# Kernel optimization log

Measured on AMD Instinct MI355X. Metric: run time of the kernel, lower is better.

The kernel has to match this reference:

```python
import jax, jax.numpy as jnp
import numpy as np

B, V, D, H, A = 512, 64, 32, 64, 8  # batch, num_vars, input_dim, hidden, out_dim
E = V * (V - 1)
HALF_LOG_2PI = 0.5 * float(np.log(2.0 * np.pi))
LOG2 = float(np.log(2.0))


def setup_inputs() -> dict:
    key = jax.random.key(0)
    ks = jax.random.split(key, 16)
    adj = np.ones((V, V)) - np.eye(V)
    send, recv = np.where(adj)
    s = 0.05
    return {
        "inputs": jax.random.normal(ks[0], (B, V, D), jnp.float32),
        "edges": jax.random.uniform(ks[1], (B, E, 2), jnp.float32),
        "m1_w": jax.random.normal(ks[2], (2 * D, H), jnp.float32) * s,
        "m1_b": jax.random.normal(ks[3], (H,), jnp.float32) * s,
        "m2_w": jax.random.normal(ks[4], (H, H), jnp.float32) * s,
        "m2_b": jax.random.normal(ks[5], (H,), jnp.float32) * s,
        "fc1_w": jax.random.normal(ks[6], (D + H, H), jnp.float32) * s,
        "fc1_b": jax.random.normal(ks[7], (H,), jnp.float32) * s,
        "fc2_w": jax.random.normal(ks[8], (H, H), jnp.float32) * s,
        "fc2_b": jax.random.normal(ks[9], (H,), jnp.float32) * s,
        "mu_w": jax.random.normal(ks[10], (H, A), jnp.float32) * 0.003,
        "mu_b": jax.random.normal(ks[11], (A,), jnp.float32) * 0.003,
        "ls_w": jax.random.normal(ks[12], (H, A), jnp.float32) * s,
        "ls_b": jax.random.normal(ks[13], (A,), jnp.float32) * s,
        "send_e": jnp.asarray(send, jnp.int32),
        "recv_e": jnp.asarray(recv, jnp.int32),
    }


def reference(inputs, edges, m1_w, m1_b, m2_w, m2_b, fc1_w, fc1_b,
              fc2_w, fc2_b, mu_w, mu_b, ls_w, ls_b, send_e, recv_e):
    # --- GNN message passing (eval mode: dropout p=0; skip edge type 0) ---
    pre_msg = jnp.concatenate(
        [inputs[:, recv_e, :], inputs[:, send_e, :]], axis=-1)  # [B,E,2D]
    h = jax.nn.relu(pre_msg @ m1_w + m1_b)                      # [B,E,H]
    msg = jax.nn.relu(h @ m2_w + m2_b) * edges[:, :, 1:2]       # [B,E,H]
    # edge2node onehot matmul == scatter-sum over receiver index
    agg = jnp.zeros((inputs.shape[0], inputs.shape[1], msg.shape[-1]),
                    msg.dtype).at[:, recv_e, :].add(msg)        # [B,V,H]
    aug = jnp.concatenate([inputs, agg], axis=-1)               # [B,V,D+H]
    # --- Policy head (eval: pi_action = mu) ---
    h1 = jax.nn.relu(aug @ fc1_w + fc1_b)
    h2 = jax.nn.relu(h1 @ fc2_w + fc2_b)
    mu = h2 @ mu_w + mu_b                                       # [B,V,A]
    log_std = jnp.clip(h2 @ ls_w + ls_b, -3.0, 1.0)
    # Normal(mu, std).log_prob(mu) = -log(std) - 0.5*log(2*pi)
    logp = jnp.sum(-log_std - HALF_LOG_2PI, axis=-1)            # [B,V]
    logp = logp - jnp.sum(
        2.0 * (LOG2 - mu - jax.nn.softplus(-2.0 * mu)), axis=-1)
    return jnp.tanh(mu), logp, aug
```

## Files before the change

kernel.cpp:

```cpp
#include <hip/hip_runtime.h>

#define NB 512
#define NV 64
#define ND 32
#define NH 64
#define NE 4032

typedef short s16x8 __attribute__((ext_vector_type(8)));
typedef float f32x4 __attribute__((ext_vector_type(4)));
typedef unsigned int u32;

#define HLOG2PI 0.9189385332046727f
#define LOG2C   0.6931471805599453f

__device__ __forceinline__ unsigned short f2bf(float f){
  u32 u = __float_as_uint(f);
  u += 0x7FFFu + ((u >> 16) & 1u);
  return (unsigned short)(u >> 16);
}
__device__ __forceinline__ u32 pk2(float a, float b){
  return (u32)f2bf(a) | ((u32)f2bf(b) << 16);
}
__device__ __forceinline__ void gload16(const void* g, void* l){
  __builtin_amdgcn_global_load_lds(
      (const __attribute__((address_space(1))) void*)g,
      (__attribute__((address_space(3))) void*)l, 16, 0, 0);
}


__global__ __launch_bounds__(256) void k_setup(
    const int* __restrict__ recv, const int* __restrict__ send,
    const float* __restrict__ x,
    const float* __restrict__ m1w, const float* __restrict__ m2w,
    const float* __restrict__ f1w, const float* __restrict__ f2w,
    const float* __restrict__ muw, const float* __restrict__ lsw,
    int* __restrict__ ebyv, int* __restrict__ sbyv,
    unsigned short* __restrict__ Wg, unsigned short* __restrict__ Fg,
    uint4* __restrict__ xbf)
{
  const int blk = blockIdx.x, t = threadIdx.x;
  if (blk == 0){
    __shared__ int cnt[NV];
    if (t < NV) cnt[t] = 0;
    __syncthreads();
    for (int e = t; e < NE; e += 256){
      int v = recv[e];
      int p = atomicAdd(&cnt[v], 1);
      ebyv[v*64 + p] = e;
      sbyv[v*64 + p] = send[e];
    }
    __syncthreads();
    if (t < NV){
      for (int s = cnt[t]; s < 64; s++){ ebyv[t*64 + s] = -1; sbyv[t*64 + s] = t; }
    }
  } else if (blk == 1){
    #pragma unroll
    for (int i = 0; i < 16; i++){ int idx = i*256 + t; int k = idx>>6, j = idx&63;
      Wg[j*64 + (((k>>3)^(j&7))<<3) + (k&7)] = f2bf(m1w[idx]); }
  } else if (blk == 2){
    #pragma unroll
    for (int i = 0; i < 16; i++){ int idx = i*256 + t; int k = idx>>6, j = idx&63;
      Wg[4096 + j*64 + (((k>>3)^(j&7))<<3) + (k&7)] = f2bf(m2w[idx]); }
  } else if (blk == 3){
    #pragma unroll
    for (int i = 0; i < 24; i++){ int idx = i*256 + t; int k = idx>>6, j = idx&63;
      Fg[j*128 + (((k>>3)^(j&7))<<3) + (k&7)] = f2bf(f1w[idx]); }
  } else if (blk == 4){
    #pragma unroll
    for (int i = 0; i < 16; i++){ int idx = i*256 + t; int k = idx>>6, j = idx&63;
      Fg[8192 + j*64 + (((k>>3)^(j&7))<<3) + (k&7)] = f2bf(f2w[idx]); }
  } else if (blk == 5){
    #pragma unroll
    for (int i = 0; i < 4; i++){ int idx = i*256 + t; int k = idx>>4, j = idx&15;
      float s = (j < 8) ? muw[k*8 + j] : lsw[k*8 + (j-8)];
      Fg[12288 + j*64 + (((k>>3)^(j&7))<<3) + (k&7)] = f2bf(s); }
  } else {
    int i = (blk - 6)*256 + t;
    const float4* s = (const float4*)x + i*2;
    float4 a = s[0], b = s[1];
    xbf[i] = make_uint4(pk2(a.x,a.y), pk2(a.z,a.w), pk2(b.x,b.y), pk2(b.z,b.w));
  }
}


__global__ __launch_bounds__(256, 3) void k_msg(
    const unsigned short* __restrict__ xbf, const float* __restrict__ x,
    const float* __restrict__ edges,
    const int* __restrict__ ebyv, const int* __restrict__ sbyv,
    const unsigned short* __restrict__ Wg,
    const float* __restrict__ b1g, const float* __restrict__ b2g,
    float* __restrict__ out_aug)
{
  __shared__ __align__(16) unsigned short Wl[2*4096];
  __shared__ __align__(16) unsigned short A[4*4096];
  __shared__ float wrow[4][64];
  __shared__ float agg[4][64];

  const int tid = threadIdx.x;
  const int w = tid >> 6, lane = tid & 63;
  const int l16 = lane & 15, l4 = lane >> 4;
  const int v = blockIdx.x & 63, bg = blockIdx.x >> 6;
  const int b = bg*4 + w;

  {
    char* lb = (char*)Wl + w*64*16;
    #pragma unroll
    for (int i = 0; i < 4; i++)
      gload16(Wg + (i*256 + tid)*8, lb + i*256*16);
  }
  {
    int e = ebyv[v*64 + lane];
    wrow[w][lane] = (e >= 0) ? edges[(b*NE + e)*2 + 1] : 0.0f;
  }
  {
    int r0 = tid >> 3;
    int s0 = sbyv[v*64 + r0];
    int s1 = sbyv[v*64 + r0 + 32];
    int c  = (tid & 7) ^ (r0 & 7);
    char* lb = (char*)A + w*64*16;
    #pragma unroll
    for (int i = 0; i < 8; i++){
      int sr   = (i & 1) ? s1 : s0;
      int node = (c < 4) ? v : sr;
      int ng   = (bg*4 + (i >> 1))*NV + node;
      gload16(xbf + ng*32 + (c & 3)*8, lb + i*256*16);
    }
  }
  __syncthreads();

  unsigned short* Ab = A + w*4096;
  const int sw = l16 & 7;

  f32x4 acc1[4][4] = {};
  #pragma unroll
  for (int ks = 0; ks < 2; ks++){
    int ch = ((ks*4 + l4) ^ sw) << 3;
    s16x8 af[4], bf[4];
    #pragma unroll
    for (int jm = 0; jm < 4; jm++) af[jm] = *(const s16x8*)(Wl + (jm*16 + l16)*64 + ch);
    #pragma unroll
    for (int il = 0; il < 4; il++) bf[il] = *(const s16x8*)(Ab + (il*16 + l16)*64 + ch);
    #pragma unroll
    for (int jm = 0; jm < 4; jm++)
      #pragma unroll
      for (int il = 0; il < 4; il++)
        acc1[jm][il] = __builtin_amdgcn_mfma_f32_16x16x32_bf16(af[jm], bf[il], acc1[jm][il], 0, 0, 0);
  }
  #pragma unroll
  for (int jm = 0; jm < 4; jm++){
    float4 bq = *(const float4*)(b1g + jm*16 + l4*4);
    int cj = jm*2 + (l4 >> 1);
    #pragma unroll
    for (int il = 0; il < 4; il++){
      float h0 = fmaxf(acc1[jm][il][0] + bq.x, 0.0f);
      float h1 = fmaxf(acc1[jm][il][1] + bq.y, 0.0f);
      float h2 = fmaxf(acc1[jm][il][2] + bq.z, 0.0f);
      float h3 = fmaxf(acc1[jm][il][3] + bq.w, 0.0f);
      int i = il*16 + l16;
      *(uint2*)(Ab + i*64 + ((cj ^ (i & 7)) << 3) + (l4 & 1)*4) =
          make_uint2(pk2(h0,h1), pk2(h2,h3));
    }
  }
  f32x4 acc2[4][4] = {};
  #pragma unroll
  for (int ks = 0; ks < 2; ks++){
    int ch = ((ks*4 + l4) ^ sw) << 3;
    s16x8 af[4], bf[4];
    #pragma unroll
    for (int im = 0; im < 4; im++) af[im] = *(const s16x8*)(Ab + (im*16 + l16)*64 + ch);
    #pragma unroll
    for (int jt = 0; jt < 4; jt++) bf[jt] = *(const s16x8*)(Wl + 4096 + (jt*16 + l16)*64 + ch);
    #pragma unroll
    for (int im = 0; im < 4; im++)
      #pragma unroll
      for (int jt = 0; jt < 4; jt++)
        acc2[im][jt] = __builtin_amdgcn_mfma_f32_16x16x32_bf16(af[im], bf[jt], acc2[im][jt], 0, 0, 0);
  }
  {
    float4 wq[4];
    #pragma unroll
    for (int im = 0; im < 4; im++) wq[im] = *(const float4*)&wrow[w][im*16 + l4*4];
    #pragma unroll
    for (int jt = 0; jt < 4; jt++){
      float b2v = b2g[jt*16 + l16];
      float s = 0.0f;
      #pragma unroll
      for (int im = 0; im < 4; im++){
        s += fmaxf(acc2[im][jt][0] + b2v, 0.0f) * wq[im].x;
        s += fmaxf(acc2[im][jt][1] + b2v, 0.0f) * wq[im].y;
        s += fmaxf(acc2[im][jt][2] + b2v, 0.0f) * wq[im].z;
        s += fmaxf(acc2[im][jt][3] + b2v, 0.0f) * wq[im].w;
      }
      s += __shfl_xor(s, 16);
      s += __shfl_xor(s, 32);
      if (l4 == 0) agg[w][jt*16 + l16] = s;
    }
  }
  {
    int rowg = b*NV + v;
    out_aug[rowg*96 + 32 + lane] = agg[w][lane];
    if (lane < 32) out_aug[rowg*96 + lane] = x[rowg*ND + lane];
  }
}


__global__ __launch_bounds__(256) void k_node(
    const float* __restrict__ aug,
    const unsigned short* __restrict__ Fg,
    const float* __restrict__ f1b, const float* __restrict__ f2b,
    const float* __restrict__ mub, const float* __restrict__ lsb,
    float* __restrict__ out0, float* __restrict__ out1)
{
  __shared__ __align__(16) unsigned short A [32*128];
  __shared__ __align__(16) unsigned short H1[32*64];
  __shared__ __align__(16) unsigned short H2[32*64];
  __shared__ __align__(16) unsigned short Wn[1664*8];
  unsigned short* F1 = Wn;
  unsigned short* F2 = Wn + 8192;
  unsigned short* HW = Wn + 12288;

  const int tid = threadIdx.x;
  const int w = tid >> 6, lane = tid & 63;
  const int l16 = lane & 15, l4 = lane >> 4;
  const int g = blockIdx.x;

  {
    char* lb = (char*)Wn + w*64*16;
    #pragma unroll
    for (int i = 0; i < 7; i++){
      if (i*256 + w*64 < 1664)
        gload16(Fg + (i*256 + w*64 + lane)*8, lb + i*256*16);
    }
  }
  #pragma unroll
  for (int i = 0; i < 2; i++){
    int c = i*256 + tid;
    if (c < 384){
      int row = (c*683) >> 13;
      int cc = c - row*12;
      const float4* s = (const float4*)(aug + (g*32 + row)*96 + cc*8);
      float4 a = s[0], bq = s[1];
      *(uint4*)(A + row*128 + ((cc ^ (row & 7)) << 3)) =
          make_uint4(pk2(a.x,a.y), pk2(a.z,a.w), pk2(bq.x,bq.y), pk2(bq.z,bq.w));
    }
  }
  __syncthreads();

  const int it = w & 1, jb = (w >> 1) * 32;
  const int irow = it*16 + l16;
  const int sw = l16 & 7;

  float f1v[2][4], f2v[2][4];
  #pragma unroll
  for (int t = 0; t < 2; t++)
    #pragma unroll
    for (int r = 0; r < 4; r++){
      f1v[t][r] = f1b[jb + t*16 + l4*4 + r];
      f2v[t][r] = f2b[jb + t*16 + l4*4 + r];
    }

  f32x4 acc[2] = {};
  #pragma unroll
  for (int ks = 0; ks < 3; ks++){
    int ch = ((ks*4 + l4) ^ sw) << 3;
    s16x8 bfrag = *(const s16x8*)(A + irow*128 + ch);
    #pragma unroll
    for (int t = 0; t < 2; t++){
      s16x8 afrag = *(const s16x8*)(F1 + (jb + t*16 + l16)*128 + ch);
      acc[t] = __builtin_amdgcn_mfma_f32_16x16x32_bf16(afrag, bfrag, acc[t], 0, 0, 0);
    }
  }
  {
    int off0 = irow*64 + (l4 & 1)*4;
    #pragma unroll
    for (int t = 0; t < 2; t++){
      float h0 = fmaxf(acc[t][0] + f1v[t][0], 0.0f);
      float h1 = fmaxf(acc[t][1] + f1v[t][1], 0.0f);
      float h2 = fmaxf(acc[t][2] + f1v[t][2], 0.0f);
      float h3 = fmaxf(acc[t][3] + f1v[t][3], 0.0f);
      int j0 = jb + t*16 + l4*4;
      *(uint2*)(H1 + off0 + (((j0 >> 3) ^ (irow & 7)) << 3)) =
          make_uint2(pk2(h0,h1), pk2(h2,h3));
    }
  }
  __syncthreads();

  f32x4 acc2[2] = {};
  #pragma unroll
  for (int ks = 0; ks < 2; ks++){
    int ch = ((ks*4 + l4) ^ sw) << 3;
    s16x8 bfrag = *(const s16x8*)(H1 + irow*64 + ch);
    #pragma unroll
    for (int t = 0; t < 2; t++){
      s16x8 afrag = *(const s16x8*)(F2 + (jb + t*16 + l16)*64 + ch);
      acc2[t] = __builtin_amdgcn_mfma_f32_16x16x32_bf16(afrag, bfrag, acc2[t], 0, 0, 0);
    }
  }
  {
    int off0 = irow*64 + (l4 & 1)*4;
    #pragma unroll
    for (int t = 0; t < 2; t++){
      float h0 = fmaxf(acc2[t][0] + f2v[t][0], 0.0f);
      float h1 = fmaxf(acc2[t][1] + f2v[t][1], 0.0f);
      float h2 = fmaxf(acc2[t][2] + f2v[t][2], 0.0f);
      float h3 = fmaxf(acc2[t][3] + f2v[t][3], 0.0f);
      int j0 = jb + t*16 + l4*4;
      *(uint2*)(H2 + off0 + (((j0 >> 3) ^ (irow & 7)) << 3)) =
          make_uint2(pk2(h0,h1), pk2(h2,h3));
    }
  }
  __syncthreads();

  if (w < 2){
    const int ir = w*16 + l16;
    f32x4 acc3 = {};
    #pragma unroll
    for (int ks = 0; ks < 2; ks++){
      int ch = ((ks*4 + l4) ^ sw) << 3;
      s16x8 a = *(const s16x8*)(H2 + ir*64 + ch);
      s16x8 bb = *(const s16x8*)(HW + l16*64 + ch);
      acc3 = __builtin_amdgcn_mfma_f32_16x16x32_bf16(a, bb, acc3, 0, 0, 0);
    }
    float bias = (l16 < 8) ? mub[l16] : lsb[l16 - 8];
    float term[4];
    #pragma unroll
    for (int r = 0; r < 4; r++){
      int grow = g*32 + w*16 + l4*4 + r;
      float val = acc3[r] + bias;
      if (l16 < 8){
        out0[grow*8 + l16] = tanhf(val);
        float xm = -2.0f * val;
        float sp = fmaxf(xm, 0.0f) + log1pf(expf(-fabsf(xm)));
        term[r] = -2.0f * (LOG2C - val - sp);
      } else {
        float lsv = fminf(fmaxf(val, -3.0f), 1.0f);
        term[r] = -lsv - HLOG2PI;
      }
    }
    #pragma unroll
    for (int r = 0; r < 4; r++){
      term[r] += __shfl_xor(term[r], 1);
      term[r] += __shfl_xor(term[r], 2);
      term[r] += __shfl_xor(term[r], 4);
      term[r] += __shfl_xor(term[r], 8);
    }
    if (l16 == 0){
      #pragma unroll
      for (int r = 0; r < 4; r++) out1[g*32 + w*16 + l4*4 + r] = term[r];
    }
  }
}


extern "C" void kernel_launch(void* const* d_in, const int* in_sizes, int n_in,
                              void* d_out, int out_size, void* d_ws, size_t ws_size,
                              hipStream_t stream) {
  const float* x     = (const float*)d_in[0];
  const float* edges = (const float*)d_in[1];
  const float* m1w   = (const float*)d_in[2];
  const float* m1b   = (const float*)d_in[3];
  const float* m2w   = (const float*)d_in[4];
  const float* m2b   = (const float*)d_in[5];
  const float* f1w   = (const float*)d_in[6];
  const float* f1b   = (const float*)d_in[7];
  const float* f2w   = (const float*)d_in[8];
  const float* f2b   = (const float*)d_in[9];
  const float* muw   = (const float*)d_in[10];
  const float* mub   = (const float*)d_in[11];
  const float* lsw   = (const float*)d_in[12];
  const float* lsb   = (const float*)d_in[13];
  const int*   send  = (const int*)d_in[14];
  const int*   recv  = (const int*)d_in[15];

  char* ws = (char*)d_ws;
  int* ebyv = (int*)ws;
  int* sbyv = (int*)(ws + 16384);
  unsigned short* Wg  = (unsigned short*)(ws + 32768);
  unsigned short* Fg  = (unsigned short*)(ws + 49152);
  unsigned short* xbf = (unsigned short*)(ws + 75776);

  float* out0    = (float*)d_out;
  float* out1    = out0 + NB*NV*8;
  float* out_aug = out1 + NB*NV;

  k_setup<<<6 + NB*NV*ND/2048, 256, 0, stream>>>(recv, send, x, m1w, m2w,
                                                 f1w, f2w, muw, lsw,
                                                 ebyv, sbyv, Wg, Fg, (uint4*)xbf);
  k_msg<<<NB*NV/4, 256, 0, stream>>>(xbf, x, edges, ebyv, sbyv, Wg,
                                     m1b, m2b, out_aug);
  k_node<<<NB*NV/32, 256, 0, stream>>>(out_aug, Fg, f1b, f2b, mub, lsb, out0, out1);
}
```

Before: 178.1 us.

## Hoist receiver-side first-layer matmul into per-node bias and restructure node kernel

The message kernel now computes the receiver half of the first message-MLP layer once per (batch, node) as an fp32 dot product folded into an effective bias. This halves the per-edge K dimension of the first MFMA, and sender rows are loaded straight into registers instead of staged through LDS. The first layer is split into two halves interleaved with the second matmul through a small per-wave LDS buffer. The node kernel is rewritten so each wave owns 16 rows end to end, loading aug directly into registers, removing block-level syncs and doubling rows per block. The risks are the scalar fp32 dot loop of 32 global loads per thread and a higher register footprint.

```diff
diff --git a/kernel.cpp b/kernel.cpp
--- a/kernel.cpp
+++ b/kernel.cpp
@@ -55,12 +55,12 @@
     }
   } else if (blk == 1){
     #pragma unroll
+    for (int i = 0; i < 8; i++){ int idx = i*256 + t; int kk = idx>>6, j = idx&63;
+      Wg[j*32 + (((kk>>3) ^ ((j>>1)&3))<<3) + (kk&7)] = f2bf(m1w[(32+kk)*64 + j]); }
+  } else if (blk == 2){
+    #pragma unroll
     for (int i = 0; i < 16; i++){ int idx = i*256 + t; int k = idx>>6, j = idx&63;
-      Wg[j*64 + (((k>>3)^(j&7))<<3) + (k&7)] = f2bf(m1w[idx]); }
-  } else if (blk == 2){
-    #pragma unroll
-    for (int i = 0; i < 16; i++){ int idx = i*256 + t; int k = idx>>6, j = idx&63;
-      Wg[4096 + j*64 + (((k>>3)^(j&7))<<3) + (k&7)] = f2bf(m2w[idx]); }
+      Wg[2048 + j*64 + (((k>>3)^(j&7))<<3) + (k&7)] = f2bf(m2w[idx]); }
   } else if (blk == 3){
     #pragma unroll
     for (int i = 0; i < 24; i++){ int idx = i*256 + t; int k = idx>>6, j = idx&63;
@@ -87,13 +87,14 @@
     const unsigned short* __restrict__ xbf, const float* __restrict__ x,
     const float* __restrict__ edges,
     const int* __restrict__ ebyv, const int* __restrict__ sbyv,
-    const unsigned short* __restrict__ Wg,
+    const unsigned short* __restrict__ Wg, const float* __restrict__ m1w,
     const float* __restrict__ b1g, const float* __restrict__ b2g,
     float* __restrict__ out_aug)
 {
-  __shared__ __align__(16) unsigned short Wl[2*4096];
-  __shared__ __align__(16) unsigned short A[4*4096];
-  __shared__ float wrow[4][64];
+  __shared__ __align__(16) unsigned short WlA[6144];
+  __shared__ __align__(16) char Hx[4][4096];
+  __shared__ float wrowS[4][64];
+  __shared__ float b1e[4][64];
   __shared__ float agg[4][64];
 
   const int tid = threadIdx.x;
@@ -102,84 +103,78 @@
   const int v = blockIdx.x & 63, bg = blockIdx.x >> 6;
   const int b = bg*4 + w;
 
-  {
-    char* lb = (char*)Wl + w*64*16;
-    #pragma unroll
-    for (int i = 0; i < 4; i++)
-      gload16(Wg + (i*256 + tid)*8, lb + i*256*16);
-  }
-  {
-    int e = ebyv[v*64 + lane];
-    wrow[w][lane] = (e >= 0) ? edges[(b*NE + e)*2 + 1] : 0.0f;
-  }
-  {
-    int r0 = tid >> 3;
-    int s0 = sbyv[v*64 + r0];
-    int s1 = sbyv[v*64 + r0 + 32];
-    int c  = (tid & 7) ^ (r0 & 7);
-    char* lb = (char*)A + w*64*16;
-    #pragma unroll
-    for (int i = 0; i < 8; i++){
-      int sr   = (i & 1) ? s1 : s0;
-      int node = (c < 4) ? v : sr;
-      int ng   = (bg*4 + (i >> 1))*NV + node;
-      gload16(xbf + ng*32 + (c & 3)*8, lb + i*256*16);
-    }
-  }
+  #pragma unroll
+  for (int i = 0; i < 3; i++)
+    gload16(Wg + (i*256 + tid)*8, (char*)WlA + i*4096 + w*1024);
+
+  int sv[4];
+  #pragma unroll
+  for (int il = 0; il < 4; il++) sv[il] = sbyv[v*64 + il*16 + l16];
+  s16x8 xf[4];
+  #pragma unroll
+  for (int il = 0; il < 4; il++)
+    xf[il] = *(const s16x8*)(xbf + (b*NV + sv[il])*32 + l4*8);
+
+  { int e = ebyv[v*64 + lane];
+    wrowS[w][lane] = (e >= 0) ? edges[(b*NE + e)*2 + 1] : 0.0f; }
+
+  { float s = b1g[lane];
+    const float* xr = x + (b*NV + v)*ND;
+    #pragma unroll
+    for (int k = 0; k < 32; k++) s = fmaf(xr[k], m1w[k*64 + lane], s);
+    b1e[w][lane] = s; }
+
   __syncthreads();
 
-  unsigned short* Ab = A + w*4096;
-  const int sw = l16 & 7;
-
-  f32x4 acc1[4][4] = {};
-  #pragma unroll
-  for (int ks = 0; ks < 2; ks++){
-    int ch = ((ks*4 + l4) ^ sw) << 3;
-    s16x8 af[4], bf[4];
-    #pragma unroll
-    for (int jm = 0; jm < 4; jm++) af[jm] = *(const s16x8*)(Wl + (jm*16 + l16)*64 + ch);
-    #pragma unroll
-    for (int il = 0; il < 4; il++) bf[il] = *(const s16x8*)(Ab + (il*16 + l16)*64 + ch);
-    #pragma unroll
-    for (int jm = 0; jm < 4; jm++)
+  const int ch32 = (l4 ^ ((l16 >> 1) & 3)) << 3;
+  const int sw8  = l16 & 7;
+  char* Hw = Hx[w];
+  const unsigned short* Wl2 = WlA + 2048;
+
+  f32x4 acc2[4][4] = {};
+  #pragma unroll
+  for (int half = 0; half < 2; half++){
+    f32x4 a1[2][4] = {};
+    #pragma unroll
+    for (int jm = 0; jm < 2; jm++){
+      s16x8 af = *(const s16x8*)(WlA + ((half*2 + jm)*16 + l16)*32 + ch32);
       #pragma unroll
       for (int il = 0; il < 4; il++)
-        acc1[jm][il] = __builtin_amdgcn_mfma_f32_16x16x32_bf16(af[jm], bf[il], acc1[jm][il], 0, 0, 0);
-  }
-  #pragma unroll
-  for (int jm = 0; jm < 4; jm++){
-    float4 bq = *(const float4*)(b1g + jm*16 + l4*4);
-    int cj = jm*2 + (l4 >> 1);
-    #pragma unroll
-    for (int il = 0; il < 4; il++){
-      float h0 = fmaxf(acc1[jm][il][0] + bq.x, 0.0f);
-      float h1 = fmaxf(acc1[jm][il][1] + bq.y, 0.0f);
-      float h2 = fmaxf(acc1[jm][il][2] + bq.z, 0.0f);
-      float h3 = fmaxf(acc1[jm][il][3] + bq.w, 0.0f);
-      int i = il*16 + l16;
-      *(uint2*)(Ab + i*64 + ((cj ^ (i & 7)) << 3) + (l4 & 1)*4) =
-          make_uint2(pk2(h0,h1), pk2(h2,h3));
-    }
-  }
-  f32x4 acc2[4][4] = {};
-  #pragma unroll
-  for (int ks = 0; ks < 2; ks++){
-    int ch = ((ks*4 + l4) ^ sw) << 3;
-    s16x8 af[4], bf[4];
-    #pragma unroll
-    for (int im = 0; im < 4; im++) af[im] = *(const s16x8*)(Ab + (im*16 + l16)*64 + ch);
-    #pragma unroll
-    for (int jt = 0; jt < 4; jt++) bf[jt] = *(const s16x8*)(Wl + 4096 + (jt*16 + l16)*64 + ch);
+        a1[jm][il] = __builtin_amdgcn_mfma_f32_16x16x32_bf16(af, xf[il], a1[jm][il], 0, 0, 0);
+    }
+    #pragma unroll
+    for (int jm = 0; jm < 2; jm++){
+      float4 bq = *(const float4*)&b1e[w][(half*2 + jm)*16 + l4*4];
+      #pragma unroll
+      for (int il = 0; il < 4; il++){
+        float h0 = fmaxf(a1[jm][il][0] + bq.x, 0.0f);
+        float h1 = fmaxf(a1[jm][il][1] + bq.y, 0.0f);
+        float h2 = fmaxf(a1[jm][il][2] + bq.z, 0.0f);
+        float h3 = fmaxf(a1[jm][il][3] + bq.w, 0.0f);
+        *(uint2*)(Hw + il*1024 + (jm*2 + (l4 >> 1))*256 + l16*16 + (l4 & 1)*8) =
+            make_uint2(pk2(h0, h1), pk2(h2, h3));
+      }
+    }
+    __builtin_amdgcn_sched_barrier(0);
+    s16x8 hf[4], wf[4];
+    #pragma unroll
+    for (int im = 0; im < 4; im++)
+      hf[im] = *(const s16x8*)(Hw + im*1024 + lane*16);
+    #pragma unroll
+    for (int jt = 0; jt < 4; jt++)
+      wf[jt] = *(const s16x8*)(Wl2 + (jt*16 + l16)*64 + (((half*4 + l4) ^ sw8) << 3));
     #pragma unroll
     for (int im = 0; im < 4; im++)
       #pragma unroll
       for (int jt = 0; jt < 4; jt++)
-        acc2[im][jt] = __builtin_amdgcn_mfma_f32_16x16x32_bf16(af[im], bf[jt], acc2[im][jt], 0, 0, 0);
-  }
+        acc2[im][jt] = __builtin_amdgcn_mfma_f32_16x16x32_bf16(hf[im], wf[jt], acc2[im][jt], 0, 0, 0);
+    __builtin_amdgcn_sched_barrier(0);
+  }
+
   {
     float4 wq[4];
     #pragma unroll
-    for (int im = 0; im < 4; im++) wq[im] = *(const float4*)&wrow[w][im*16 + l4*4];
+    for (int im = 0; im < 4; im++) wq[im] = *(const float4*)&wrowS[w][im*16 + l4*4];
     #pragma unroll
     for (int jt = 0; jt < 4; jt++){
       float b2v = b2g[jt*16 + l16];
@@ -196,6 +191,7 @@
       if (l4 == 0) agg[w][jt*16 + l16] = s;
     }
   }
+  __builtin_amdgcn_sched_barrier(0);
   {
     int rowg = b*NV + v;
     out_aug[rowg*96 + 32 + lane] = agg[w][lane];
@@ -211,144 +207,109 @@
     const float* __restrict__ mub, const float* __restrict__ lsb,
     float* __restrict__ out0, float* __restrict__ out1)
 {
-  __shared__ __align__(16) unsigned short A [32*128];
-  __shared__ __align__(16) unsigned short H1[32*64];
-  __shared__ __align__(16) unsigned short H2[32*64];
   __shared__ __align__(16) unsigned short Wn[1664*8];
-  unsigned short* F1 = Wn;
-  unsigned short* F2 = Wn + 8192;
-  unsigned short* HW = Wn + 12288;
+  __shared__ __align__(16) char Hn[4][2048];
+  const unsigned short* F1 = Wn;
+  const unsigned short* F2 = Wn + 8192;
+  const unsigned short* HW = Wn + 12288;
 
   const int tid = threadIdx.x;
   const int w = tid >> 6, lane = tid & 63;
   const int l16 = lane & 15, l4 = lane >> 4;
-  const int g = blockIdx.x;
-
-  {
-    char* lb = (char*)Wn + w*64*16;
-    #pragma unroll
-    for (int i = 0; i < 7; i++){
-      if (i*256 + w*64 < 1664)
-        gload16(Fg + (i*256 + w*64 + lane)*8, lb + i*256*16);
-    }
-  }
-  #pragma unroll
-  for (int i = 0; i < 2; i++){
-    int c = i*256 + tid;
-    if (c < 384){
-      int row = (c*683) >> 13;
-      int cc = c - row*12;
-      const float4* s = (const float4*)(aug + (g*32 + row)*96 + cc*8);
-      float4 a = s[0], bq = s[1];
-      *(uint4*)(A + row*128 + ((cc ^ (row & 7)) << 3)) =
-          make_uint4(pk2(a.x,a.y), pk2(a.z,a.w), pk2(bq.x,bq.y), pk2(bq.z,bq.w));
-    }
+  const int row = blockIdx.x*64 + w*16 + l16;
+
+  #pragma unroll
+  for (int i = 0; i < 7; i++){
+    if (i*256 + w*64 < 1664)
+      gload16(Fg + (i*256 + w*64 + lane)*8, (char*)Wn + i*4096 + w*1024);
+  }
+  s16x8 bf1[3];
+  #pragma unroll
+  for (int ks = 0; ks < 3; ks++){
+    const float4* p = (const float4*)(aug + row*96 + (ks*4 + l4)*8);
+    float4 a = p[0], c = p[1];
+    union { uint4 q; s16x8 v; } uu;
+    uu.q = make_uint4(pk2(a.x,a.y), pk2(a.z,a.w), pk2(c.x,c.y), pk2(c.z,c.w));
+    bf1[ks] = uu.v;
   }
   __syncthreads();
 
-  const int it = w & 1, jb = (w >> 1) * 32;
-  const int irow = it*16 + l16;
-  const int sw = l16 & 7;
-
-  float f1v[2][4], f2v[2][4];
-  #pragma unroll
-  for (int t = 0; t < 2; t++)
+  const int sw8 = l16 & 7;
+  char* Hw = Hn[w];
+
+  f32x4 a1[4] = {};
+  #pragma unroll
+  for (int ks = 0; ks < 3; ks++)
+    #pragma unroll
+    for (int jt = 0; jt < 4; jt++){
+      s16x8 af = *(const s16x8*)(F1 + (jt*16 + l16)*128 + (((ks*4 + l4) ^ sw8) << 3));
+      a1[jt] = __builtin_amdgcn_mfma_f32_16x16x32_bf16(af, bf1[ks], a1[jt], 0, 0, 0);
+    }
+  #pragma unroll
+  for (int jt = 0; jt < 4; jt++){
+    float4 bq = *(const float4*)(f1b + jt*16 + l4*4);
+    float h0 = fmaxf(a1[jt][0] + bq.x, 0.0f);
+    float h1 = fmaxf(a1[jt][1] + bq.y, 0.0f);
+    float h2 = fmaxf(a1[jt][2] + bq.z, 0.0f);
+    float h3 = fmaxf(a1[jt][3] + bq.w, 0.0f);
+    *(uint2*)(Hw + (jt >> 1)*1024 + ((jt & 1)*2 + (l4 >> 1))*256 + l16*16 + (l4 & 1)*8) =
+        make_uint2(pk2(h0, h1), pk2(h2, h3));
+  }
+  __builtin_amdgcn_sched_barrier(0);
+  s16x8 bh[2];
+  bh[0] = *(const s16x8*)(Hw + lane*16);
+  bh[1] = *(const s16x8*)(Hw + 1024 + lane*16);
+  f32x4 a2[4] = {};
+  #pragma unroll
+  for (int ks = 0; ks < 2; ks++)
+    #pragma unroll
+    for (int jt = 0; jt < 4; jt++){
+      s16x8 af = *(const s16x8*)(F2 + (jt*16 + l16)*64 + (((ks*4 + l4) ^ sw8) << 3));
+      a2[jt] = __builtin_amdgcn_mfma_f32_16x16x32_bf16(af, bh[ks], a2[jt], 0, 0, 0);
+    }
+  __builtin_amdgcn_sched_barrier(0);
+  #pragma unroll
+  for (int jt = 0; jt < 4; jt++){
+    float4 bq = *(const float4*)(f2b + jt*16 + l4*4);
+    float h0 = fmaxf(a2[jt][0] + bq.x, 0.0f);
+    float h1 = fmaxf(a2[jt][1] + bq.y, 0.0f);
+    float h2 = fmaxf(a2[jt][2] + bq.z, 0.0f);
+    float h3 = fmaxf(a2[jt][3] + bq.w, 0.0f);
+    *(uint2*)(Hw + (jt >> 1)*1024 + ((jt & 1)*2 + (l4 >> 1))*256 + l16*16 + (l4 & 1)*8) =
+        make_uint2(pk2(h0, h1), pk2(h2, h3));
+  }
+  __builtin_amdgcn_sched_barrier(0);
+  bh[0] = *(const s16x8*)(Hw + lane*16);
+  bh[1] = *(const s16x8*)(Hw + 1024 + lane*16);
+  f32x4 a3 = {};
+  #pragma unroll
+  for (int ks = 0; ks < 2; ks++){
+    s16x8 af = *(const s16x8*)(HW + l16*64 + (((ks*4 + l4) ^ sw8) << 3));
+    a3 = __builtin_amdgcn_mfma_f32_16x16x32_bf16(af, bh[ks], a3, 0, 0, 0);
+  }
+  float term = 0.0f;
+  if (l4 < 2){
+    float4 t;
     #pragma unroll
     for (int r = 0; r < 4; r++){
-      f1v[t][r] = f1b[jb + t*16 + l4*4 + r];
-      f2v[t][r] = f2b[jb + t*16 + l4*4 + r];
-    }
-
-  f32x4 acc[2] = {};
-  #pragma unroll
-  for (int ks = 0; ks < 3; ks++){
-    int ch = ((ks*4 + l4) ^ sw) << 3;
-    s16x8 bfrag = *(const s16x8*)(A + irow*128 + ch);
-    #pragma unroll
-    for (int t = 0; t < 2; t++){
-      s16x8 afrag = *(const s16x8*)(F1 + (jb + t*16 + l16)*128 + ch);
-      acc[t] = __builtin_amdgcn_mfma_f32_16x16x32_bf16(afrag, bfrag, acc[t], 0, 0, 0);
-    }
-  }
-  {
-    int off0 = irow*64 + (l4 & 1)*4;
-    #pragma unroll
-    for (int t = 0; t < 2; t++){
-      float h0 = fmaxf(acc[t][0] + f1v[t][0], 0.0f);
-      float h1 = fmaxf(acc[t][1] + f1v[t][1], 0.0f);
-      float h2 = fmaxf(acc[t][2] + f1v[t][2], 0.0f);
-      float h3 = fmaxf(acc[t][3] + f1v[t][3], 0.0f);
-      int j0 = jb + t*16 + l4*4;
-      *(uint2*)(H1 + off0 + (((j0 >> 3) ^ (irow & 7)) << 3)) =
-          make_uint2(pk2(h0,h1), pk2(h2,h3));
-    }
-  }
-  __syncthreads();
-
-  f32x4 acc2[2] = {};
-  #pragma unroll
-  for (int ks = 0; ks < 2; ks++){
-    int ch = ((ks*4 + l4) ^ sw) << 3;
-    s16x8 bfrag = *(const s16x8*)(H1 + irow*64 + ch);
-    #pragma unroll
-    for (int t = 0; t < 2; t++){
-      s16x8 afrag = *(const s16x8*)(F2 + (jb + t*16 + l16)*64 + ch);
-      acc2[t] = __builtin_amdgcn_mfma_f32_16x16x32_bf16(afrag, bfrag, acc2[t], 0, 0, 0);
-    }
-  }
-  {
-    int off0 = irow*64 + (l4 & 1)*4;
-    #pragma unroll
-    for (int t = 0; t < 2; t++){
-      float h0 = fmaxf(acc2[t][0] + f2v[t][0], 0.0f);
-      float h1 = fmaxf(acc2[t][1] + f2v[t][1], 0.0f);
-      float h2 = fmaxf(acc2[t][2] + f2v[t][2], 0.0f);
-      float h3 = fmaxf(acc2[t][3] + f2v[t][3], 0.0f);
-      int j0 = jb + t*16 + l4*4;
-      *(uint2*)(H2 + off0 + (((j0 >> 3) ^ (irow & 7)) << 3)) =
-          make_uint2(pk2(h0,h1), pk2(h2,h3));
-    }
-  }
-  __syncthreads();
-
-  if (w < 2){
-    const int ir = w*16 + l16;
-    f32x4 acc3 = {};
-    #pragma unroll
-    for (int ks = 0; ks < 2; ks++){
-      int ch = ((ks*4 + l4) ^ sw) << 3;
-      s16x8 a = *(const s16x8*)(H2 + ir*64 + ch);
-      s16x8 bb = *(const s16x8*)(HW + l16*64 + ch);
-      acc3 = __builtin_amdgcn_mfma_f32_16x16x32_bf16(a, bb, acc3, 0, 0, 0);
-    }
-    float bias = (l16 < 8) ? mub[l16] : lsb[l16 - 8];
-    float term[4];
+      int o = l4*4 + r;
+      float mu = a3[r] + mub[o];
+      ((float*)&t)[r] = tanhf(mu);
+      float xm = -2.0f * mu;
+      float sp = fmaxf(xm, 0.0f) + log1pf(expf(-fabsf(xm)));
+      term += -2.0f * (LOG2C - mu - sp);
+    }
+    *(float4*)(out0 + row*8 + l4*4) = t;
+  } else {
     #pragma unroll
     for (int r = 0; r < 4; r++){
-      int grow = g*32 + w*16 + l4*4 + r;
-      float val = acc3[r] + bias;
-      if (l16 < 8){
-        out0[grow*8 + l16] = tanhf(val);
-        float xm = -2.0f * val;
-        float sp = fmaxf(xm, 0.0f) + log1pf(expf(-fabsf(xm)));
-        term[r] = -2.0f * (LOG2C - val - sp);
-      } else {
-        float lsv = fminf(fmaxf(val, -3.0f), 1.0f);
-        term[r] = -lsv - HLOG2PI;
-      }
-    }
-    #pragma unroll
-    for (int r = 0; r < 4; r++){
-      term[r] += __shfl_xor(term[r], 1);
-      term[r] += __shfl_xor(term[r], 2);
-      term[r] += __shfl_xor(term[r], 4);
-      term[r] += __shfl_xor(term[r], 8);
-    }
-    if (l16 == 0){
-      #pragma unroll
-      for (int r = 0; r < 4; r++) out1[g*32 + w*16 + l4*4 + r] = term[r];
-    }
-  }
+      float lsv = fminf(fmaxf(a3[r] + lsb[l4*4 + r - 8], -3.0f), 1.0f);
+      term += -lsv - HLOG2PI;
+    }
+  }
+  term += __shfl_xor(term, 16);
+  term += __shfl_xor(term, 32);
+  if (l4 == 0) out1[row] = term;
 }
 
 
@@ -386,7 +347,7 @@
   k_setup<<<6 + NB*NV*ND/2048, 256, 0, stream>>>(recv, send, x, m1w, m2w,
                                                  f1w, f2w, muw, lsw,
                                                  ebyv, sbyv, Wg, Fg, (uint4*)xbf);
-  k_msg<<<NB*NV/4, 256, 0, stream>>>(xbf, x, edges, ebyv, sbyv, Wg,
+  k_msg<<<NB*NV/4, 256, 0, stream>>>(xbf, x, edges, ebyv, sbyv, Wg, m1w,
                                      m1b, m2b, out_aug);
-  k_node<<<NB*NV/32, 256, 0, stream>>>(out_aug, Fg, f1b, f2b, mub, lsb, out0, out1);
-}
+  k_node<<<NB*NV/64, 256, 0, stream>>>(out_aug, Fg, f1b, f2b, mub, lsb, out0, out1);
+}
```

After: 163.9 us. 8.0% less time.
